# Kernel optimization log

Hardware: AMD Instinct MI355X
Metric: run time of the kernel (lower is better)

Reference implementation:

```python
import jax, jax.numpy as jnp
import numpy as np

B, S, E, H = 8, 1024, 1024, 16
D = E // H  # head_dim = 64


def setup_inputs() -> dict:
    key = jax.random.key(0)
    ks = jax.random.split(key, 10)
    def lin(k):
        kw, kb = jax.random.split(k)
        lim = 1.0 / np.sqrt(E)
        W = jax.random.uniform(kw, (E, E), jnp.float32, -lim, lim)
        b = jax.random.uniform(kb, (E,), jnp.float32, -lim, lim)
        return W, b
    Wq, bq = lin(ks[0]); Wk, bk = lin(ks[1]); Wv, bv = lin(ks[2]); Wo, bo = lin(ks[3])
    ent = jax.random.normal(ks[4], (H, H), jnp.float32)
    x = jax.random.normal(ks[5], (B, S, E), jnp.float32)
    mask = jnp.ones((B, 1, S, S), jnp.int32)
    return {"x": x, "mask": mask, "Wq": Wq, "bq": bq, "Wk": Wk, "bk": bk,
            "Wv": Wv, "bv": bv, "Wo": Wo, "bo": bo, "ent": ent}


def reference(x, mask, Wq, bq, Wk, bk, Wv, bv, Wo, bo, ent):
    Bs, Sl, Ed = x.shape
    def heads(W, b):
        return (x @ W.T + b).reshape(Bs, Sl, H, D).transpose(0, 2, 1, 3)  # [B,H,S,D]
    q, k, v = heads(Wq, bq), heads(Wk, bk), heads(Wv, bv)
    scores = jnp.einsum('bhqd,bhkd->bhqk', q, k) / np.sqrt(D)  # [B,H,S,S]
    Em = jax.nn.softmax(ent, axis=-1)  # [H,H]
    scores = jnp.einsum('bhqk,hg->bgqk', scores, Em)  # cross-head entanglement mix
    scores = jnp.where(mask == 0, jnp.float32(-1e9), scores)
    attn = jax.nn.softmax(scores, axis=-1)
    out = jnp.einsum('bhqk,bhkd->bhqd', attn, v)
    out = out.transpose(0, 2, 1, 3).reshape(Bs, Sl, Ed)
    return out @ Wo.T + bo
```

## Files before the change

### kernel.cpp

```cpp
#include <hip/hip_runtime.h>

#define DEVINL static __device__ __forceinline__

typedef __attribute__((ext_vector_type(4)))  float f32x4;
typedef __attribute__((ext_vector_type(16))) float f32x16;
typedef __attribute__((ext_vector_type(4)))  float float4_t;
typedef __attribute__((ext_vector_type(8)))  short short8;
typedef __attribute__((ext_vector_type(4)))  short short4v;
typedef __attribute__((ext_vector_type(4)))  int   int4v;
typedef __attribute__((ext_vector_type(2)))  unsigned u32x2;

DEVINL unsigned short f2bf(float f){
  union { float f; unsigned int u; } x; x.f = f;
  return (unsigned short)((x.u + 0x7fffu + ((x.u >> 16) & 1u)) >> 16);
}
DEVINL float bf2f(unsigned short h){
  union { unsigned int u; float f; } x; x.u = ((unsigned int)h) << 16;
  return x.f;
}
DEVINL f32x4 zero4(){ f32x4 z; z[0]=0.f; z[1]=0.f; z[2]=0.f; z[3]=0.f; return z; }
DEVINL f32x16 zero16(){ f32x16 z;
#pragma unroll
  for (int e=0;e<16;++e) z[e]=0.f;
  return z; }

#define BARX() do{ \
  __builtin_amdgcn_sched_barrier(0); \
  asm volatile("s_waitcnt lgkmcnt(0)" ::: "memory"); \
  __builtin_amdgcn_sched_barrier(0); \
  __builtin_amdgcn_s_barrier(); \
  __builtin_amdgcn_sched_barrier(0); \
}while(0)

#define GLL16(gp, lp) __builtin_amdgcn_global_load_lds( \
    (const __attribute__((address_space(1))) void*)(gp), \
    (__attribute__((address_space(3))) void*)(lp), 16, 0, 0)

__global__ __launch_bounds__(256) void cast_f32_bf16(const float* __restrict__ src,
                                                     unsigned short* __restrict__ dst, int n8){
  int i = blockIdx.x * 256 + threadIdx.x;
  if (i >= n8) return;
  const float4_t* s = (const float4_t*)src;
  float4_t a = s[2*i], b = s[2*i+1];
  short8 o;
  o[0]=(short)f2bf(a[0]); o[1]=(short)f2bf(a[1]); o[2]=(short)f2bf(a[2]); o[3]=(short)f2bf(a[3]);
  o[4]=(short)f2bf(b[0]); o[5]=(short)f2bf(b[1]); o[6]=(short)f2bf(b[2]); o[7]=(short)f2bf(b[3]);
  *(short8*)(dst + (size_t)i*8) = o;
}

__global__ __launch_bounds__(256) void prep_em(const float* __restrict__ ent,
                                               unsigned short* __restrict__ EmT){
  int t = threadIdx.x;
  if (t < 16){
    float v[16]; float mx = -3.0e38f;
#pragma unroll
    for (int j=0;j<16;++j){ v[j] = ent[t*16 + j]; mx = fmaxf(mx, v[j]); }
    float s = 0.f;
#pragma unroll
    for (int j=0;j<16;++j){ v[j] = __expf(v[j]-mx); s += v[j]; }
    float inv = (1.f/s) * 0.125f * 1.4426950408889634f;
#pragma unroll
    for (int j=0;j<16;++j) EmT[j*16 + t] = f2bf(v[j]*inv);
  }
  EmT[256 + t] = 0;
}

__global__ __launch_bounds__(256) void prep_maskbits(const int* __restrict__ mask,
                                                     unsigned* __restrict__ mb){
  int id = blockIdx.x * 256 + threadIdx.x;
  const int* src = mask + (size_t)id * 32;
  unsigned word = 0u;
#pragma unroll
  for (int c=0;c<8;++c){
    int4v v = *(const int4v*)(src + c*4);
    word |= (unsigned)(v[0]!=0) << (c*4)
          | (unsigned)(v[1]!=0) << (c*4+1)
          | (unsigned)(v[2]!=0) << (c*4+2)
          | (unsigned)(v[3]!=0) << (c*4+3);
  }
  mb[id] = word;
}

template<int MODE>
__global__ __launch_bounds__(256) void gemm_bt(const unsigned short* __restrict__ A,
                                               const unsigned short* __restrict__ W4,
                                               const float* __restrict__ bias0,
                                               const float* __restrict__ bias1,
                                               const float* __restrict__ bias2,
                                               void* __restrict__ outp){
  __shared__ __align__(16) unsigned short As[4096];
  __shared__ __align__(16) unsigned short Bs[4096];
  const int tid = threadIdx.x;
  const int w = tid >> 6, ln = tid & 63;
  const int wm = w >> 1, wn = w & 1;
  const int lq = ln & 15, lg = ln >> 4;
  const int m0 = blockIdx.y * 128, n0 = blockIdx.x * 128;
  const int z = blockIdx.z;
  const unsigned short* Bt = W4 + (size_t)z * 1048576;
  const float* bias = (z == 0) ? bias0 : ((z == 1) ? bias1 : bias2);

  const unsigned short* Ag = A  + (size_t)(m0 + (tid >> 2)) * 1024 + (tid & 3) * 8;
  const unsigned short* Bg = Bt + (size_t)(n0 + (tid >> 2)) * 1024 + (tid & 3) * 8;
  unsigned short* lA0 = As + w * 512;
  unsigned short* lA1 = As + 2048 + w * 512;
  unsigned short* lB0 = Bs + w * 512;
  unsigned short* lB1 = Bs + 2048 + w * 512;

  f32x4 acc[4][4];
#pragma unroll
  for (int i=0;i<4;++i)
#pragma unroll
    for (int j=0;j<4;++j) acc[i][j] = zero4();

  for (int kb = 0; kb < 32; ++kb){
    const int k0 = kb * 32;
    GLL16(Ag + k0,         lA0);
    GLL16(Ag + k0 + 65536, lA1);
    GLL16(Bg + k0,         lB0);
    GLL16(Bg + k0 + 65536, lB1);
    __syncthreads();
    short8 af[4], bf_[4];
#pragma unroll
    for (int i=0;i<4;++i) af[i]  = *(const short8*)(As + (wm*64 + i*16 + lq)*32 + lg*8);
#pragma unroll
    for (int j=0;j<4;++j) bf_[j] = *(const short8*)(Bs + (wn*64 + j*16 + lq)*32 + lg*8);
#pragma unroll
    for (int i=0;i<4;++i)
#pragma unroll
      for (int j=0;j<4;++j)
        acc[i][j] = __builtin_amdgcn_mfma_f32_16x16x32_bf16(af[i], bf_[j], acc[i][j], 0, 0, 0);
    __syncthreads();
  }

  const int mrow = m0 + wm*64, ncol = n0 + wn*64;
  float bj[4];
#pragma unroll
  for (int j=0;j<4;++j) bj[j] = bias[ncol + j*16 + lq];
#pragma unroll
  for (int i=0;i<4;++i)
#pragma unroll
    for (int j=0;j<4;++j)
#pragma unroll
      for (int r=0;r<4;++r){
        float v = acc[i][j][r] + bj[j];
        int m = mrow + i*16 + lg*4 + r;
        int n = ncol + j*16 + lq;
        if (MODE == 0){
          int bb = m >> 10, sI = m & 1023, h = n >> 6, d = n & 63;
          ((unsigned short*)outp)[(size_t)z*8388608 + (((size_t)bb*16 + h)*1024 + sI)*64 + d] = f2bf(v);
        } else {
          ((float*)outp)[(size_t)m*1024 + n] = v;
        }
      }
}

__global__ __launch_bounds__(256) void transpose_v(const unsigned short* __restrict__ V,
                                                   unsigned short* __restrict__ Vt){
  int idx = blockIdx.x * 256 + threadIdx.x;
  int s8 = idx & 127, d = (idx >> 7) & 63, bh = idx >> 13;
  const unsigned short* src = V + (size_t)bh*65536 + (size_t)s8*8*64 + d;
  short8 o;
#pragma unroll
  for (int j=0;j<8;++j) o[j] = (short)src[(size_t)j*64];
  *(short8*)(Vt + (size_t)bh*65536 + (size_t)d*1024 + (size_t)s8*8) = o;
}

__global__ __launch_bounds__(512,2) void attn_fused(const unsigned short* __restrict__ Q,
    const unsigned short* __restrict__ K, const unsigned short* __restrict__ Vt,
    const unsigned* __restrict__ MB, const unsigned short* __restrict__ EmT,
    unsigned short* __restrict__ AO){
  __shared__ __align__(16) unsigned short sraw[16384];
  __shared__ __align__(16) unsigned short smix[16384];
  const int tid = threadIdx.x;
  const int w = tid >> 6, ln = tid & 63;
  const int lq = ln & 15, lg = ln >> 4;
  const int l5 = ln & 31, h5 = ln >> 5;
  const int bid = blockIdx.x;
  const int bb = bid & 7, q0 = (bid >> 3) * 16;
  const int aQ = w & 3, n0 = w >> 2, g0 = w * 2;

  const unsigned short* Qb = Q  + ((size_t)bb*16 + 4*aQ) * 65536;
  const unsigned short* Kb = K  + ((size_t)bb*16 + 4*aQ) * 65536 + (size_t)(n0*32 + lq)*64 + lg*8;
  const unsigned short* Vb = Vt + ((size_t)bb*16 + g0) * 65536;
  const unsigned* Mwp = MB + (size_t)bb*32768 + (size_t)(q0 + lq)*32;

  short8 emA = *(const short8*)(EmT + l5*16 + h5*8);

  short8 qf[4][2];
#pragma unroll
  for (int hh=0; hh<4; ++hh)
#pragma unroll
    for (int ks=0; ks<2; ++ks)
      qf[hh][ks] = *(const short8*)(Qb + (size_t)hh*65536 + (size_t)(q0 + lq)*64 + ks*32 + lg*8);

  f32x4 acco[2][4];
#pragma unroll
  for (int a=0;a<2;++a)
#pragma unroll
    for (int n=0;n<4;++n) acco[a][n] = zero4();
  float mst[2] = {-3.0e38f,-3.0e38f};
  float lst[2] = {0.f,0.f};

  for (int kt = 0; kt < 16; ++kt){
    const int kb = kt*64;
    const u32x2 mw = *(const u32x2*)(Mwp + kt*2);
    short8 vfr[2][4][2];
#pragma unroll
    for (int hh=0;hh<2;++hh)
#pragma unroll
      for (int n=0;n<4;++n)
#pragma unroll
        for (int kh=0;kh<2;++kh)
          vfr[hh][n][kh] = *(const short8*)(Vb + (size_t)hh*65536 + (size_t)(n*16 + lq)*1024 + kb + kh*32 + lg*8);

    f32x4 accs[4][2];
#pragma unroll
    for (int hh=0; hh<4; ++hh){
      short8 kf[2][2];
#pragma unroll
      for (int n=0;n<2;++n)
#pragma unroll
        for (int ks=0;ks<2;++ks)
          kf[n][ks] = *(const short8*)(Kb + (size_t)hh*65536 + (size_t)(kb + n*16)*64 + ks*32);
#pragma unroll
      for (int n=0;n<2;++n){
        accs[hh][n] = __builtin_amdgcn_mfma_f32_16x16x32_bf16(qf[hh][0], kf[n][0], zero4(), 0,0,0);
        accs[hh][n] = __builtin_amdgcn_mfma_f32_16x16x32_bf16(qf[hh][1], kf[n][1], accs[hh][n], 0,0,0);
      }
    }
#pragma unroll
    for (int n=0;n<2;++n)
#pragma unroll
      for (int r=0;r<4;++r){
        const int qq = lg*4 + r;
        const int kk = n0*32 + n*16 + lq;
        short4v pk;
        pk[0]=(short)f2bf(accs[0][n][r]); pk[1]=(short)f2bf(accs[1][n][r]);
        pk[2]=(short)f2bf(accs[2][n][r]); pk[3]=(short)f2bf(accs[3][n][r]);
        const int lin = (qq*64 + kk)*32 + aQ*8;
        const int sw  = (((kk>>2)&1)<<4) | (((qq>>2)&3)<<5);
        *(short4v*)((char*)sraw + (lin ^ sw)) = pk;
      }
    BARX();
#pragma unroll
    for (int t=0;t<4;++t){
      const int qq = w*2 + (t&1);
      const int kh = t>>1;
      const int kk = kh*32 + l5;
      const int lin = (qq*64 + kk)*32 + h5*16;
      const int sw  = (((kk>>2)&1)<<4) | (((qq>>2)&3)<<5);
      short8 sfr = *(const short8*)((const char*)sraw + (lin ^ sw));
      f32x16 md = __builtin_amdgcn_mfma_f32_32x32x16_bf16(emA, sfr, zero16(), 0,0,0);
#pragma unroll
      for (int reg=0;reg<8;++reg){
        const int gg = (reg&3) + 8*(reg>>2) + 4*h5;
        int ob = gg*2048 + qq*128 + kk*2;
        ob ^= ((qq&7)<<4) ^ (((gg>>2)&1)<<6);
        *(short*)((char*)smix + ob) = (short)f2bf(md[reg]);
      }
    }
    BARX();
    const unsigned mb0 = (mw[0] >> (lg*8)) & 0xffu;
    const unsigned mb1 = (mw[1] >> (lg*8)) & 0xffu;
    const int allon = __all((int)((mb0 & mb1) == 0xffu));
#pragma unroll
    for (int hh=0; hh<2; ++hh){
      const int gg = g0 + hh;
      const int swc = ((lq&7)<<4) ^ (((gg>>2)&1)<<6);
      const int base = gg*2048 + lq*128 + lg*16;
      short8 sm0 = *(const short8*)((const char*)smix + ((base      ) ^ swc));
      short8 sm1 = *(const short8*)((const char*)smix + ((base + 64 ) ^ swc));
      float s[16];
#pragma unroll
      for (int j=0;j<8;++j){ s[j] = bf2f((unsigned short)sm0[j]); s[8+j] = bf2f((unsigned short)sm1[j]); }
      if (!allon){
#pragma unroll
        for (int j=0;j<8;++j){
          if (!((mb0>>j)&1u)) s[j]    = -1.44269504e9f;
          if (!((mb1>>j)&1u)) s[8+j]  = -1.44269504e9f;
        }
      }
      float m01 = fmaxf(s[0],s[1]),  m23 = fmaxf(s[2],s[3]);
      float m45 = fmaxf(s[4],s[5]),  m67 = fmaxf(s[6],s[7]);
      float m89 = fmaxf(s[8],s[9]),  mab = fmaxf(s[10],s[11]);
      float mcd = fmaxf(s[12],s[13]),mef = fmaxf(s[14],s[15]);
      float pm = fmaxf(fmaxf(fmaxf(m01,m23), fmaxf(m45,m67)),
                       fmaxf(fmaxf(m89,mab), fmaxf(mcd,mef)));
      pm = fmaxf(pm, __shfl_xor(pm, 16, 64));
      pm = fmaxf(pm, __shfl_xor(pm, 32, 64));
      const float mo = mst[hh];
      const float mn = fmaxf(mo, pm);
      const float sc = exp2f(mo - mn);
      float p[16];
#pragma unroll
      for (int j=0;j<16;++j) p[j] = exp2f(s[j] - mn);
      float ps = 0.f;
#pragma unroll
      for (int j=0;j<16;++j) ps += p[j];
      ps += __shfl_xor(ps, 16, 64);
      ps += __shfl_xor(ps, 32, 64);
      lst[hh] = lst[hh]*sc + ps;
      mst[hh] = mn;
      short8 pa0, pa1;
#pragma unroll
      for (int j=0;j<8;++j){ pa0[j] = (short)f2bf(p[j]); pa1[j] = (short)f2bf(p[8+j]); }
#pragma unroll
      for (int n=0;n<4;++n){
        acco[hh][n][0] *= sc; acco[hh][n][1] *= sc;
        acco[hh][n][2] *= sc; acco[hh][n][3] *= sc;
      }
#pragma unroll
      for (int n=0;n<4;++n){
        acco[hh][n] = __builtin_amdgcn_mfma_f32_16x16x32_bf16(vfr[hh][n][0], pa0, acco[hh][n], 0,0,0);
        acco[hh][n] = __builtin_amdgcn_mfma_f32_16x16x32_bf16(vfr[hh][n][1], pa1, acco[hh][n], 0,0,0);
      }
    }
  }
#pragma unroll
  for (int hh=0; hh<2; ++hh){
    const int gg = g0 + hh;
    const float linv = 1.0f / lst[hh];
    const size_t rowb = ((size_t)(bb*1024 + q0 + lq))*2048;
#pragma unroll
    for (int n=0;n<4;++n){
      unsigned w0 = (unsigned)f2bf(acco[hh][n][0]*linv) | ((unsigned)f2bf(acco[hh][n][1]*linv) << 16);
      unsigned w1 = (unsigned)f2bf(acco[hh][n][2]*linv) | ((unsigned)f2bf(acco[hh][n][3]*linv) << 16);
      const int e = gg*64 + n*16 + lg*4;
      *(unsigned*)((char*)AO + rowb + (size_t)e*2    ) = w0;
      *(unsigned*)((char*)AO + rowb + (size_t)e*2 + 4) = w1;
    }
  }
}

extern "C" void kernel_launch(void* const* d_in, const int* in_sizes, int n_in,
                              void* d_out, int out_size, void* d_ws, size_t ws_size,
                              hipStream_t stream){
  const float* x   = (const float*)d_in[0];
  const int*   msk = (const int*)  d_in[1];
  const float* Wq  = (const float*)d_in[2];
  const float* bq  = (const float*)d_in[3];
  const float* Wk  = (const float*)d_in[4];
  const float* bk  = (const float*)d_in[5];
  const float* Wv  = (const float*)d_in[6];
  const float* bv  = (const float*)d_in[7];
  const float* Wo  = (const float*)d_in[8];
  const float* bo  = (const float*)d_in[9];
  const float* ent = (const float*)d_in[10];

  char* ws = (char*)d_ws;
  unsigned short* xb  = (unsigned short*)(ws);
  unsigned short* Wb  = (unsigned short*)(ws + 16777216);
  unsigned short* qkv = (unsigned short*)(ws + 25165824);
  unsigned short* EmT = (unsigned short*)(ws + 75497472);
  unsigned*       MB  = (unsigned*)     (ws + 75499520);
  unsigned short* Vt  = xb;
  unsigned short* AO  = qkv + (size_t)2*8388608;

  cast_f32_bf16<<<4096, 256, 0, stream>>>(x,  xb,            1048576);
  cast_f32_bf16<<<512,  256, 0, stream>>>(Wq, Wb,            131072);
  cast_f32_bf16<<<512,  256, 0, stream>>>(Wk, Wb + 1048576,  131072);
  cast_f32_bf16<<<512,  256, 0, stream>>>(Wv, Wb + 2097152,  131072);
  cast_f32_bf16<<<512,  256, 0, stream>>>(Wo, Wb + 3145728,  131072);
  prep_em<<<1, 256, 0, stream>>>(ent, EmT);
  prep_maskbits<<<1024, 256, 0, stream>>>(msk, MB);

  gemm_bt<0><<<dim3(8,64,3), 256, 0, stream>>>(xb, Wb, bq, bk, bv, (void*)qkv);
  transpose_v<<<4096, 256, 0, stream>>>(qkv + (size_t)2*8388608, Vt);
  attn_fused<<<512, 512, 0, stream>>>(qkv, qkv + 8388608, Vt, MB, EmT, AO);
  gemm_bt<1><<<dim3(8,64,1), 256, 0, stream>>>(AO, Wb + 3145728, bo, bo, bo, d_out);

  (void)in_sizes; (void)n_in; (void)out_size; (void)ws_size;
}
```

Baseline: 436.7 us.

## Double-buffer score tiles to prefetch next QK^T and use packed bf16 conversion

Splits the QK^T score computation into a helper and computes the next key tile's scores into a second LDS buffer while the current tile's head-mix and softmax run, removing one block barrier per iteration. Also replaces the manual round-to-nearest bf16 conversion with HIP's packed float2-to-bfloat162 intrinsic in the cast kernel, the score packing, the probability packing and the output store. Doubling the sraw/smix buffers doubles the kernel's LDS footprint, which may lower the number of resident blocks per CU and raises register pressure from the prefetched accumulators.

After: 432.9 us. No clear change (-0.9%).

```diff
diff --git a/kernel.cpp b/kernel.cpp
--- a/kernel.cpp
+++ b/kernel.cpp
@@ -1,4 +1,5 @@
 #include <hip/hip_runtime.h>
+#include <hip/hip_bf16.h>
 
 #define DEVINL static __device__ __forceinline__
 
@@ -9,10 +10,15 @@
 typedef __attribute__((ext_vector_type(4)))  short short4v;
 typedef __attribute__((ext_vector_type(4)))  int   int4v;
 typedef __attribute__((ext_vector_type(2)))  unsigned u32x2;
+typedef __attribute__((ext_vector_type(4)))  unsigned u32x4;
 
 DEVINL unsigned short f2bf(float f){
-  union { float f; unsigned int u; } x; x.f = f;
-  return (unsigned short)((x.u + 0x7fffu + ((x.u >> 16) & 1u)) >> 16);
+  __hip_bfloat16 h = __float2bfloat16(f);
+  unsigned short u; __builtin_memcpy(&u, &h, 2); return u;
+}
+DEVINL unsigned pk2(float lo, float hi){
+  __hip_bfloat162 h2 = __float22bfloat162_rn(make_float2(lo, hi));
+  unsigned u; __builtin_memcpy(&u, &h2, 4); return u;
 }
 DEVINL float bf2f(unsigned short h){
   union { unsigned int u; float f; } x; x.u = ((unsigned int)h) << 16;
@@ -42,10 +48,10 @@
   if (i >= n8) return;
   const float4_t* s = (const float4_t*)src;
   float4_t a = s[2*i], b = s[2*i+1];
-  short8 o;
-  o[0]=(short)f2bf(a[0]); o[1]=(short)f2bf(a[1]); o[2]=(short)f2bf(a[2]); o[3]=(short)f2bf(a[3]);
-  o[4]=(short)f2bf(b[0]); o[5]=(short)f2bf(b[1]); o[6]=(short)f2bf(b[2]); o[7]=(short)f2bf(b[3]);
-  *(short8*)(dst + (size_t)i*8) = o;
+  u32x4 o;
+  o[0]=pk2(a[0],a[1]); o[1]=pk2(a[2],a[3]);
+  o[2]=pk2(b[0],b[1]); o[3]=pk2(b[2],b[3]);
+  *(u32x4*)(dst + (size_t)i*8) = o;
 }
 
 __global__ __launch_bounds__(256) void prep_em(const float* __restrict__ ent,
@@ -169,8 +175,8 @@
     const unsigned short* __restrict__ K, const unsigned short* __restrict__ Vt,
     const unsigned* __restrict__ MB, const unsigned short* __restrict__ EmT,
     unsigned short* __restrict__ AO){
-  __shared__ __align__(16) unsigned short sraw[16384];
-  __shared__ __align__(16) unsigned short smix[16384];
+  __shared__ __align__(16) unsigned short sraw[2][16384];
+  __shared__ __align__(16) unsigned short smix[2][16384];
   const int tid = threadIdx.x;
   const int w = tid >> 6, ln = tid & 63;
   const int lq = ln & 15, lg = ln >> 4;
@@ -201,7 +207,43 @@
   float mst[2] = {-3.0e38f,-3.0e38f};
   float lst[2] = {0.f,0.f};
 
+  auto QKT = [&](int KT, unsigned short* dst){
+    const int kb = KT*64;
+    f32x4 accs[4][2];
+#pragma unroll
+    for (int hh=0; hh<4; ++hh){
+      short8 kf[2][2];
+#pragma unroll
+      for (int n=0;n<2;++n)
+#pragma unroll
+        for (int ks=0;ks<2;++ks)
+          kf[n][ks] = *(const short8*)(Kb + (size_t)hh*65536 + (size_t)(kb + n*16)*64 + ks*32);
+#pragma unroll
+      for (int n=0;n<2;++n){
+        accs[hh][n] = __builtin_amdgcn_mfma_f32_16x16x32_bf16(qf[hh][0], kf[n][0], zero4(), 0,0,0);
+        accs[hh][n] = __builtin_amdgcn_mfma_f32_16x16x32_bf16(qf[hh][1], kf[n][1], accs[hh][n], 0,0,0);
+      }
+    }
+#pragma unroll
+    for (int n=0;n<2;++n)
+#pragma unroll
+      for (int r=0;r<4;++r){
+        const int qq = lg*4 + r;
+        const int kk = n0*32 + n*16 + lq;
+        u32x2 pk;
+        pk[0] = pk2(accs[0][n][r], accs[1][n][r]);
+        pk[1] = pk2(accs[2][n][r], accs[3][n][r]);
+        const int lin = (qq*64 + kk)*32 + aQ*8;
+        const int sw  = (((kk>>2)&1)<<4) | (((qq>>2)&3)<<5);
+        *(u32x2*)((char*)dst + (lin ^ sw)) = pk;
+      }
+  };
+
+  QKT(0, &sraw[0][0]);
+  BARX();
+
   for (int kt = 0; kt < 16; ++kt){
+    const int buf = kt & 1;
     const int kb = kt*64;
     const u32x2 mw = *(const u32x2*)(Mwp + kt*2);
     short8 vfr[2][4][2];
@@ -213,35 +255,8 @@
         for (int kh=0;kh<2;++kh)
           vfr[hh][n][kh] = *(const short8*)(Vb + (size_t)hh*65536 + (size_t)(n*16 + lq)*1024 + kb + kh*32 + lg*8);
 
-    f32x4 accs[4][2];
-#pragma unroll
-    for (int hh=0; hh<4; ++hh){
-      short8 kf[2][2];
-#pragma unroll
-      for (int n=0;n<2;++n)
-#pragma unroll
-        for (int ks=0;ks<2;++ks)
-          kf[n][ks] = *(const short8*)(Kb + (size_t)hh*65536 + (size_t)(kb + n*16)*64 + ks*32);
-#pragma unroll
-      for (int n=0;n<2;++n){
-        accs[hh][n] = __builtin_amdgcn_mfma_f32_16x16x32_bf16(qf[hh][0], kf[n][0], zero4(), 0,0,0);
-        accs[hh][n] = __builtin_amdgcn_mfma_f32_16x16x32_bf16(qf[hh][1], kf[n][1], accs[hh][n], 0,0,0);
-      }
-    }
-#pragma unroll
-    for (int n=0;n<2;++n)
-#pragma unroll
-      for (int r=0;r<4;++r){
-        const int qq = lg*4 + r;
-        const int kk = n0*32 + n*16 + lq;
-        short4v pk;
-        pk[0]=(short)f2bf(accs[0][n][r]); pk[1]=(short)f2bf(accs[1][n][r]);
-        pk[2]=(short)f2bf(accs[2][n][r]); pk[3]=(short)f2bf(accs[3][n][r]);
-        const int lin = (qq*64 + kk)*32 + aQ*8;
-        const int sw  = (((kk>>2)&1)<<4) | (((qq>>2)&3)<<5);
-        *(short4v*)((char*)sraw + (lin ^ sw)) = pk;
-      }
-    BARX();
+    if (kt < 15) QKT(kt+1, &sraw[buf^1][0]);
+
 #pragma unroll
     for (int t=0;t<4;++t){
       const int qq = w*2 + (t&1);
@@ -249,14 +264,14 @@
       const int kk = kh*32 + l5;
       const int lin = (qq*64 + kk)*32 + h5*16;
       const int sw  = (((kk>>2)&1)<<4) | (((qq>>2)&3)<<5);
-      short8 sfr = *(const short8*)((const char*)sraw + (lin ^ sw));
+      short8 sfr = *(const short8*)((const char*)&sraw[buf][0] + (lin ^ sw));
       f32x16 md = __builtin_amdgcn_mfma_f32_32x32x16_bf16(emA, sfr, zero16(), 0,0,0);
 #pragma unroll
       for (int reg=0;reg<8;++reg){
         const int gg = (reg&3) + 8*(reg>>2) + 4*h5;
         int ob = gg*2048 + qq*128 + kk*2;
         ob ^= ((qq&7)<<4) ^ (((gg>>2)&1)<<6);
-        *(short*)((char*)smix + ob) = (short)f2bf(md[reg]);
+        *(short*)((char*)&smix[buf][0] + ob) = (short)f2bf(md[reg]);
       }
     }
     BARX();
@@ -268,8 +283,8 @@
       const int gg = g0 + hh;
       const int swc = ((lq&7)<<4) ^ (((gg>>2)&1)<<6);
       const int base = gg*2048 + lq*128 + lg*16;
-      short8 sm0 = *(const short8*)((const char*)smix + ((base      ) ^ swc));
-      short8 sm1 = *(const short8*)((const char*)smix + ((base + 64 ) ^ swc));
+      short8 sm0 = *(const short8*)((const char*)&smix[buf][0] + ((base      ) ^ swc));
+      short8 sm1 = *(const short8*)((const char*)&smix[buf][0] + ((base + 64 ) ^ swc));
       float s[16];
 #pragma unroll
       for (int j=0;j<8;++j){ s[j] = bf2f((unsigned short)sm0[j]); s[8+j] = bf2f((unsigned short)sm1[j]); }
@@ -301,9 +316,11 @@
       ps += __shfl_xor(ps, 32, 64);
       lst[hh] = lst[hh]*sc + ps;
       mst[hh] = mn;
-      short8 pa0, pa1;
-#pragma unroll
-      for (int j=0;j<8;++j){ pa0[j] = (short)f2bf(p[j]); pa1[j] = (short)f2bf(p[8+j]); }
+      union { short8 s8; u32x4 u4; } pa0, pa1;
+      pa0.u4[0]=pk2(p[0],p[1]);   pa0.u4[1]=pk2(p[2],p[3]);
+      pa0.u4[2]=pk2(p[4],p[5]);   pa0.u4[3]=pk2(p[6],p[7]);
+      pa1.u4[0]=pk2(p[8],p[9]);   pa1.u4[1]=pk2(p[10],p[11]);
+      pa1.u4[2]=pk2(p[12],p[13]); pa1.u4[3]=pk2(p[14],p[15]);
 #pragma unroll
       for (int n=0;n<4;++n){
         acco[hh][n][0] *= sc; acco[hh][n][1] *= sc;
@@ -311,8 +328,8 @@
       }
 #pragma unroll
       for (int n=0;n<4;++n){
-        acco[hh][n] = __builtin_amdgcn_mfma_f32_16x16x32_bf16(vfr[hh][n][0], pa0, acco[hh][n], 0,0,0);
-        acco[hh][n] = __builtin_amdgcn_mfma_f32_16x16x32_bf16(vfr[hh][n][1], pa1, acco[hh][n], 0,0,0);
+        acco[hh][n] = __builtin_amdgcn_mfma_f32_16x16x32_bf16(vfr[hh][n][0], pa0.s8, acco[hh][n], 0,0,0);
+        acco[hh][n] = __builtin_amdgcn_mfma_f32_16x16x32_bf16(vfr[hh][n][1], pa1.s8, acco[hh][n], 0,0,0);
       }
     }
   }
@@ -323,8 +340,8 @@
     const size_t rowb = ((size_t)(bb*1024 + q0 + lq))*2048;
 #pragma unroll
     for (int n=0;n<4;++n){
-      unsigned w0 = (unsigned)f2bf(acco[hh][n][0]*linv) | ((unsigned)f2bf(acco[hh][n][1]*linv) << 16);
-      unsigned w1 = (unsigned)f2bf(acco[hh][n][2]*linv) | ((unsigned)f2bf(acco[hh][n][3]*linv) << 16);
+      unsigned w0 = pk2(acco[hh][n][0]*linv, acco[hh][n][1]*linv);
+      unsigned w1 = pk2(acco[hh][n][2]*linv, acco[hh][n][3]*linv);
       const int e = gg*64 + n*16 + lg*4;
       *(unsigned*)((char*)AO + rowb + (size_t)e*2    ) = w0;
       *(unsigned*)((char*)AO + rowb + (size_t)e*2 + 4) = w1;
```
